# Optimization experiments

Measured on AMD Instinct MI355X. Metric: run time of the kernel, lower is better.

The kernel has to match this reference:

```python
import jax, jax.numpy as jnp
import numpy as np

B, N, NCLS = 32, 8732, 20           # batch, anchors, scored classes (bg excluded)
CONF_T, IOU_T = 0.01, 0.45
TOP_K, NMS_MAX = 200, 100
IMG_H = IMG_W = 512.0


def setup_inputs() -> dict:
    key = jax.random.key(0)
    y_pred = jax.random.uniform(key, (B, N, NCLS + 13), dtype=jnp.float32)
    return {"y_pred": y_pred}


def _decode(y):
    # SSD box decode: offsets + anchors + variances -> absolute corner coords
    scores = y[..., 1:-12]                                  # [B,N,C]
    cx_p, cy_p, w_p, h_p = y[..., -12], y[..., -11], y[..., -10], y[..., -9]
    xmin_a, ymin_a, xmax_a, ymax_a = y[..., -8], y[..., -7], y[..., -6], y[..., -5]
    w_a, h_a = xmax_a - xmin_a, ymax_a - ymin_a
    cx_a, cy_a = (xmax_a + xmin_a) * 0.5, (ymax_a + ymin_a) * 0.5
    vcx, vcy, vw, vh = y[..., -4], y[..., -3], y[..., -2], y[..., -1]
    cx = cx_p * vcx * w_a + cx_a
    cy = cy_p * vcy * h_a + cy_a
    w = jnp.exp(w_p * vw) * w_a
    h = jnp.exp(h_p * vh) * h_a
    xmin = (cx - 0.5 * w) * IMG_W
    ymin = (cy - 0.5 * h) * IMG_H
    xmax = (cx + 0.5 * w) * IMG_W
    ymax = (cy + 0.5 * h) * IMG_H
    boxes = jnp.stack([xmin, ymin, xmax, ymax], axis=-1)    # [B,N,4]
    return boxes, scores


def _select(boxes, scores):
    # Greedy per-class NMS. boxes [N,4], scores [N] (-inf below threshold).
    # Returns (indices into original box order, validity) of length NMS_MAX.
    n = scores.shape[0]
    order = jnp.argsort(-scores)
    b = boxes[order]
    s = scores[order]
    area = jnp.maximum(b[:, 2] - b[:, 0], 0.0) * jnp.maximum(b[:, 3] - b[:, 1], 0.0)
    idx_range = jnp.arange(n)

    def step(suppressed, _):
        avail = (~suppressed) & (s > -jnp.inf)
        i = jnp.argmax(avail)            # first unsuppressed box in score order
        has = avail[i]
        box = b[i]
        ix1 = jnp.maximum(box[0], b[:, 0])
        iy1 = jnp.maximum(box[1], b[:, 1])
        ix2 = jnp.minimum(box[2], b[:, 2])
        iy2 = jnp.minimum(box[3], b[:, 3])
        inter = jnp.maximum(ix2 - ix1, 0.0) * jnp.maximum(iy2 - iy1, 0.0)
        iou = inter / (area[i] + area - inter + 1e-9)
        suppressed = suppressed | (has & (iou > IOU_T)) | (idx_range == i)
        return suppressed, (order[i], has)

    _, (sel, valid) = jax.lax.scan(step, jnp.zeros(n, bool), None, length=NMS_MAX)
    return sel, valid


def _forward(y_pred):
    boxes, scores = _decode(y_pred)                          # [B,N,4], [B,N,C]
    s_thr = jnp.where(scores > CONF_T, scores, -jnp.inf)
    s_bcn = jnp.transpose(s_thr, (0, 2, 1))                  # [B,C,N]
    # NMS selection is index-only: run it on stop_gradient'd values
    sel, valid = jax.vmap(jax.vmap(_select, in_axes=(None, 0)), in_axes=(0, 0))(
        jax.lax.stop_gradient(boxes), jax.lax.stop_gradient(s_bcn))  # [B,C,M]
    Bv, C, M = sel.shape
    batch_ix = jnp.arange(Bv)
    sel_scores = jnp.take_along_axis(s_bcn, sel, axis=2)     # [B,C,M]
    sel_boxes = boxes[batch_ix[:, None, None], sel]          # [B,C,M,4]
    masked = jnp.where(valid, sel_scores, -jnp.inf)
    flat_s = masked.reshape(Bv, C * M)
    flat_b = sel_boxes.reshape(Bv, C * M, 4)
    flat_v = valid.reshape(Bv, C * M)
    _, top_idx = jax.lax.top_k(jax.lax.stop_gradient(flat_s), TOP_K)  # [B,TOP_K]
    g_s = jnp.take_along_axis(flat_s, top_idx, axis=1)
    g_v = jnp.take_along_axis(flat_v, top_idx, axis=1)
    g_b = flat_b[batch_ix[:, None], top_idx]                 # [B,TOP_K,4]
    cls = (top_idx // M).astype(jnp.float32)
    cls_out = jnp.where(g_v, cls, 0.0) + 1.0                 # layer does nmsed_class += 1
    score_out = jnp.where(g_v, g_s, 0.0)
    box_out = jnp.where(g_v[..., None], g_b, 0.0)
    return jnp.concatenate([cls_out[..., None], score_out[..., None], box_out], axis=-1)


def reference(y_pred):
    return _forward(y_pred)  # [B, TOP_K, 6]: [class_id, conf, xmin, ymin, xmax, ymax]
```

## Files before the change

kernel.cpp:

```cpp
#include <hip/hip_runtime.h>
#include <cmath>

#define BB 32
#define NN 8732
#define NCLS 20
#define NCH 33
#define NMSM 100
#define TOPK 200
#define CAND (NCLS*NMSM)
#define APB 256
#define NBLK_B ((NN + APB - 1)/APB)
#define NBUCK 2048
#define CCAP 256
#define CMIN 192
#define TBUCK 4096
#define TCMIN 200

typedef unsigned long long u64;
typedef unsigned int u32;

__device__ __forceinline__ u64 shfl_xor_u64(u64 v, int m) {
  u32 lo = (u32)v, hi = (u32)(v >> 32);
  lo = (u32)__shfl_xor((int)lo, m, 64);
  hi = (u32)__shfl_xor((int)hi, m, 64);
  return ((u64)hi << 32) | (u64)lo;
}

__global__ __launch_bounds__(256)
void decode_kernel(const float* __restrict__ y,
                   float4* __restrict__ boxes,
                   float* __restrict__ scores_t) {
  __shared__ float ly[APB * NCH];
  int blk = blockIdx.x;
  int b = blk / NBLK_B, chunk = blk % NBLK_B;
  int a0 = chunk * APB;
  int na = min(APB, NN - a0);
  const float4* src4 = (const float4*)(y + ((size_t)b * NN + a0) * NCH);
  float4* ly4 = (float4*)ly;
  int nf4 = na * NCH / 4;
  for (int k = threadIdx.x; k < nf4; k += 256) ly4[k] = src4[k];
  __syncthreads();
  int t = threadIdx.x;
  if (t < na) {
    const float* p = ly + t * NCH;
    #pragma unroll
    for (int c = 0; c < NCLS; c++)
      scores_t[((size_t)b * NCLS + c) * NN + a0 + t] = p[1 + c];
    float cx_p = p[21], cy_p = p[22], w_p = p[23], h_p = p[24];
    float xmin_a = p[25], ymin_a = p[26], xmax_a = p[27], ymax_a = p[28];
    float vcx = p[29], vcy = p[30], vw = p[31], vh = p[32];
    float w_a = xmax_a - xmin_a, h_a = ymax_a - ymin_a;
    float cx_a = (xmax_a + xmin_a) * 0.5f, cy_a = (ymax_a + ymin_a) * 0.5f;
    float cx = cx_p * vcx * w_a + cx_a;
    float cy = cy_p * vcy * h_a + cy_a;
    float w = expf(w_p * vw) * w_a;
    float h = expf(h_p * vh) * h_a;
    float4 bxv;
    bxv.x = (cx - 0.5f * w) * 512.0f;
    bxv.y = (cy - 0.5f * h) * 512.0f;
    bxv.z = (cx + 0.5f * w) * 512.0f;
    bxv.w = (cy + 0.5f * h) * 512.0f;
    boxes[b * NN + a0 + t] = bxv;
  }
}

__global__ __launch_bounds__(256)
void nms_kernel(const float4* __restrict__ boxes,
                const float* __restrict__ scores_t,
                float* __restrict__ sel_score,
                float4* __restrict__ sel_box) {
  __shared__ u32 hist[NBUCK];
  __shared__ u32 chunks[256];
  __shared__ u64 ckey[CCAP];
  __shared__ float4 lbox[CCAP];
  __shared__ float lar[CCAP];
  __shared__ u64 sel_k[NMSM];
  __shared__ int sel_g[NMSM];
  __shared__ int s_cnt, s_bstar, s_nsel;

  int bc = blockIdx.x, b = bc / NCLS;
  const float* sc = scores_t + (size_t)bc * NN;
  const float4* bx = boxes + (size_t)b * NN;
  int tid = threadIdx.x, lane = tid & 63, wid = tid >> 6;

  for (int k = tid; k < NBUCK; k += 256) hist[k] = 0;
  if (tid == 0) s_cnt = 0;
  __syncthreads();

  {
    const float4* sc4 = (const float4*)sc;
    for (int n = tid; n < NN / 4; n += 256) {
      float4 v = sc4[n];
      if (v.x > 0.01f) atomicAdd(&hist[min((int)(v.x * (float)NBUCK), NBUCK - 1)], 1u);
      if (v.y > 0.01f) atomicAdd(&hist[min((int)(v.y * (float)NBUCK), NBUCK - 1)], 1u);
      if (v.z > 0.01f) atomicAdd(&hist[min((int)(v.z * (float)NBUCK), NBUCK - 1)], 1u);
      if (v.w > 0.01f) atomicAdd(&hist[min((int)(v.w * (float)NBUCK), NBUCK - 1)], 1u);
    }
  }
  __syncthreads();
  {
    u32 cs = 0;
    #pragma unroll
    for (int q = 0; q < 8; q++) cs += hist[tid * 8 + q];
    chunks[tid] = cs;
  }
  __syncthreads();
  if (tid == 0) {
    int acc = 0, bstar = 0;
    for (int c2 = 255; c2 >= 0; c2--) {
      int na2 = acc + (int)chunks[c2];
      if (na2 >= CMIN) {
        for (int q = 7; q >= 0; q--) {
          acc += (int)hist[c2 * 8 + q];
          if (acc >= CMIN) { bstar = c2 * 8 + q; break; }
        }
        break;
      }
      acc = na2;
    }
    s_bstar = bstar;
  }
  __syncthreads();
  int bstar = s_bstar;

  for (int n = tid; n < NN; n += 256) {
    float s = sc[n];
    bool q = false;
    if (s > 0.01f) q = (min((int)(s * (float)NBUCK), NBUCK - 1) >= bstar);
    u64 mask = __ballot(q);
    if (mask) {
      int leader = __ffsll(mask) - 1;
      int base = 0;
      if (q && lane == leader) base = atomicAdd(&s_cnt, __popcll(mask));
      base = __shfl(base, leader);
      if (q) {
        int pos = base + __popcll(mask & ((1ULL << lane) - 1ULL));
        if (pos < CCAP)
          ckey[pos] = ((u64)__float_as_uint(s) << 32) | (u64)(0xFFFFFFFFu - (u32)n);
      }
    }
  }
  __syncthreads();
  if (tid >= min(s_cnt, CCAP)) ckey[tid] = 0ULL;
  __syncthreads();

  u64 key[4];
  if (wid == 0) {
    #pragma unroll
    for (int s = 0; s < 4; s++) key[s] = ckey[4 * lane + s];
    for (int k = 2; k <= CCAP; k <<= 1) {
      for (int j = k >> 1; j >= 4; j >>= 1) {
        int lm = j >> 2;
        #pragma unroll
        for (int s = 0; s < 4; s++) {
          u64 pk = shfl_xor_u64(key[s], lm);
          int g = 4 * lane + s;
          bool lower = (g & j) == 0;
          bool desc = (g & k) == 0;
          bool keepmax = (desc == lower);
          u64 mx = (key[s] > pk) ? key[s] : pk;
          u64 mn = (key[s] > pk) ? pk : key[s];
          key[s] = keepmax ? mx : mn;
        }
      }
      if (k >= 4) {
        #pragma unroll
        for (int s = 0; s < 2; s++) {
          int g = 4 * lane + s;
          bool desc = (g & k) == 0;
          u64 a = key[s], c2 = key[s + 2];
          u64 mx = (a > c2) ? a : c2, mn = (a > c2) ? c2 : a;
          key[s] = desc ? mx : mn; key[s + 2] = desc ? mn : mx;
        }
      }
      {
        #pragma unroll
        for (int s = 0; s < 4; s += 2) {
          int g = 4 * lane + s;
          bool desc = (g & k) == 0;
          u64 a = key[s], c2 = key[s + 1];
          u64 mx = (a > c2) ? a : c2, mn = (a > c2) ? c2 : a;
          key[s] = desc ? mx : mn; key[s + 1] = desc ? mn : mx;
        }
      }
    }
    #pragma unroll
    for (int s = 0; s < 4; s++) ckey[4 * lane + s] = key[s];
  }
  __syncthreads();

  {
    u64 g = ckey[tid];
    float4 bb = make_float4(0.f, 0.f, 0.f, 0.f);
    if (g) bb = bx[(int)(0xFFFFFFFFu - (u32)g)];
    lbox[tid] = bb;
    lar[tid] = fmaxf(bb.z - bb.x, 0.f) * fmaxf(bb.w - bb.y, 0.f);
  }
  __syncthreads();

  if (wid == 0) {
    float X1[4], Y1[4], X2[4], Y2[4], AR[4];
    u32 am = 0, dg = 0;
    #pragma unroll
    for (int s = 0; s < 4; s++) {
      int g = 4 * lane + s;
      float4 bb = lbox[g];
      X1[s] = bb.x; Y1[s] = bb.y; X2[s] = bb.z; Y2[s] = bb.w;
      AR[s] = lar[g];
      if (key[s]) am |= (1u << s);
      if (!(AR[s] > 0.f)) dg |= (1u << s);
    }
    int nsel = 0;
    #pragma unroll 1
    for (int m = 0; m < NMSM; m++) {
      u64 bal = __ballot(am != 0u);
      if (bal == 0ULL) break;
      int w = __ffsll(bal) - 1;
      int sl_ = (__ffs(am) - 1) & 3;
      u32 pk = (u32)sl_ | (((dg >> sl_) & 1u) << 2);
      u32 pkw = (u32)__shfl((int)pk, w, 64);
      int slw = (int)(pkw & 3u);
      int g = (w << 2) + slw;
      if (lane == w) {
        am &= ~(1u << slw);
        u64 kk = key[0];
        if (slw == 1) kk = key[1];
        if (slw == 2) kk = key[2];
        if (slw == 3) kk = key[3];
        sel_k[m] = kk;
        sel_g[m] = g;
      }
      nsel = m + 1;
      if ((pkw & 4u) == 0u) {
        float4 sb = lbox[g];
        float sa = lar[g];
        #pragma unroll
        for (int s = 0; s < 4; s++) {
          float ix1 = fmaxf(sb.x, X1[s]), iy1 = fmaxf(sb.y, Y1[s]);
          float ix2 = fminf(sb.z, X2[s]), iy2 = fminf(sb.w, Y2[s]);
          float inter = fmaxf(ix2 - ix1, 0.f) * fmaxf(iy2 - iy1, 0.f);
          float iou = inter / (sa + AR[s] - inter + 1e-9f);
          if (iou > 0.45f) am &= ~(1u << s);
        }
      }
    }
    if (lane == 0) s_nsel = nsel;
  }
  __syncthreads();

  int nsel = s_nsel;
  if (tid < NMSM) {
    if (tid < nsel) {
      u64 kk = sel_k[tid];
      sel_score[(size_t)bc * NMSM + tid] = __uint_as_float((u32)(kk >> 32));
      sel_box[(size_t)bc * NMSM + tid] = lbox[sel_g[tid]];
    } else {
      sel_score[(size_t)bc * NMSM + tid] = -INFINITY;
    }
  }
}

__global__ __launch_bounds__(512)
void topk_kernel(const float* __restrict__ sel_score,
                 const float4* __restrict__ sel_box,
                 float* __restrict__ out) {
  __shared__ float lsc[CAND];
  __shared__ u32 hist[TBUCK];
  __shared__ u64 ckey[512];
  __shared__ u32 chunks[512];
  __shared__ int s_cnt, s_bstar;
  int b = blockIdx.x;
  int tid = threadIdx.x;
  int lane = tid & 63;

  for (int k = tid; k < TBUCK; k += 512) hist[k] = 0;
  if (tid == 0) s_cnt = 0;
  __syncthreads();
  for (int t = tid; t < CAND; t += 512) {
    float s = sel_score[(size_t)b * CAND + t];
    lsc[t] = s;
    if (s > 0.f) atomicAdd(&hist[min((int)(s * (float)TBUCK), TBUCK - 1)], 1u);
  }
  __syncthreads();
  {
    u32 cs = 0;
    #pragma unroll
    for (int q = 0; q < 8; q++) cs += hist[tid * 8 + q];
    chunks[tid] = cs;
  }
  __syncthreads();
  if (tid == 0) {
    int acc = 0, bstar = 0;
    for (int c2 = 511; c2 >= 0; c2--) {
      int na = acc + (int)chunks[c2];
      if (na >= TCMIN) {
        for (int q = 7; q >= 0; q--) {
          acc += (int)hist[c2 * 8 + q];
          if (acc >= TCMIN) { bstar = c2 * 8 + q; break; }
        }
        break;
      }
      acc = na;
    }
    s_bstar = bstar;
  }
  __syncthreads();
  int bstar = s_bstar;
  for (int t = tid; t < CAND; t += 512) {
    float s = lsc[t];
    bool q = false;
    if (s > 0.f) q = (min((int)(s * (float)TBUCK), TBUCK - 1) >= bstar);
    u64 mask = __ballot(q);
    if (mask) {
      int leader = __ffsll(mask) - 1;
      int base = 0;
      if (q && lane == leader) base = atomicAdd(&s_cnt, __popcll(mask));
      base = __shfl(base, leader);
      if (q) {
        int pos = base + __popcll(mask & ((1ULL << lane) - 1ULL));
        if (pos < 512)
          ckey[pos] = ((u64)__float_as_uint(s) << 32) | (u64)(0xFFFFFFFFu - (u32)t);
      }
    }
  }
  __syncthreads();
  int C = min(s_cnt, 512);
  for (int k = C + tid; k < 512; k += 512) ckey[k] = 0ULL;
  __syncthreads();

  for (int kk = 2; kk <= 512; kk <<= 1) {
    for (int j = kk >> 1; j > 0; j >>= 1) {
      int t = tid;
      int ixj = t ^ j;
      if (ixj > t && t < 512) {
        u64 a = ckey[t], c2 = ckey[ixj];
        bool desc = ((t & kk) == 0);
        if (desc ? (a < c2) : (a > c2)) { ckey[t] = c2; ckey[ixj] = a; }
      }
      __syncthreads();
    }
  }

  for (int k = tid; k < TOPK; k += 512) {
    u64 g = ckey[k];
    float o0 = 1.0f, o1 = 0.0f;
    float4 bb = make_float4(0.f, 0.f, 0.f, 0.f);
    if (g != 0ULL) {
      int flat = (int)(0xFFFFFFFFu - (u32)g);
      o0 = (float)(flat / NMSM) + 1.0f;
      o1 = __uint_as_float((u32)(g >> 32));
      bb = sel_box[(size_t)b * CAND + flat];
    }
    float* op = out + ((size_t)b * TOPK + k) * 6;
    op[0] = o0; op[1] = o1; op[2] = bb.x; op[3] = bb.y; op[4] = bb.z; op[5] = bb.w;
  }
}

extern "C" void kernel_launch(void* const* d_in, const int* in_sizes, int n_in,
                              void* d_out, int out_size, void* d_ws, size_t ws_size,
                              hipStream_t stream) {
  const float* y = (const float*)d_in[0];
  float* out = (float*)d_out;
  char* ws = (char*)d_ws;

  size_t boxesB = (size_t)BB * NN * 16;
  size_t scoresB = (size_t)BB * NCLS * NN * 4;
  size_t selScoreB = (size_t)BB * CAND * 4;

  float4* boxes    = (float4*)ws;
  float* scores_t  = (float*)(ws + boxesB);
  float* sel_score = (float*)(ws + boxesB + scoresB);
  float4* sel_box  = (float4*)(ws + boxesB + scoresB + selScoreB);

  decode_kernel<<<BB * NBLK_B, 256, 0, stream>>>(y, boxes, scores_t);
  nms_kernel<<<BB * NCLS, 256, 0, stream>>>(boxes, scores_t, sel_score, sel_box);
  topk_kernel<<<BB, 512, 0, stream>>>(sel_score, sel_box, out);
}
```

Measured before the change: 143.4 us.

## Decode boxes lazily for NMS candidates and keep scores in registers

Box decoding moves out of the first kernel, so no full boxes buffer is written and read back. Each NMS block decodes boxes only for its up-to-256 candidates, reading them straight from the raw input. The score row is now loaded once into registers and reused for both the histogram and compaction passes instead of being read from global memory twice. A shfl is also replaced with readlane. In exchange, boxes are decoded redundantly across classes and per-candidate strided gathers of 12 floats are added, along with more register pressure from the 9 float4 values.

```diff
diff --git a/kernel.cpp b/kernel.cpp
--- a/kernel.cpp
+++ b/kernel.cpp
@@ -13,6 +13,7 @@
 #define NBUCK 2048
 #define CCAP 256
 #define CMIN 192
+#define NF4 (NN/4)
 #define TBUCK 4096
 #define TCMIN 200
 
@@ -27,9 +28,8 @@
 }
 
 __global__ __launch_bounds__(256)
-void decode_kernel(const float* __restrict__ y,
-                   float4* __restrict__ boxes,
-                   float* __restrict__ scores_t) {
+void transpose_kernel(const float* __restrict__ y,
+                      float* __restrict__ scores_t) {
   __shared__ float ly[APB * NCH];
   int blk = blockIdx.x;
   int b = blk / NBLK_B, chunk = blk % NBLK_B;
@@ -46,26 +46,11 @@
     #pragma unroll
     for (int c = 0; c < NCLS; c++)
       scores_t[((size_t)b * NCLS + c) * NN + a0 + t] = p[1 + c];
-    float cx_p = p[21], cy_p = p[22], w_p = p[23], h_p = p[24];
-    float xmin_a = p[25], ymin_a = p[26], xmax_a = p[27], ymax_a = p[28];
-    float vcx = p[29], vcy = p[30], vw = p[31], vh = p[32];
-    float w_a = xmax_a - xmin_a, h_a = ymax_a - ymin_a;
-    float cx_a = (xmax_a + xmin_a) * 0.5f, cy_a = (ymax_a + ymin_a) * 0.5f;
-    float cx = cx_p * vcx * w_a + cx_a;
-    float cy = cy_p * vcy * h_a + cy_a;
-    float w = expf(w_p * vw) * w_a;
-    float h = expf(h_p * vh) * h_a;
-    float4 bxv;
-    bxv.x = (cx - 0.5f * w) * 512.0f;
-    bxv.y = (cy - 0.5f * h) * 512.0f;
-    bxv.z = (cx + 0.5f * w) * 512.0f;
-    bxv.w = (cy + 0.5f * h) * 512.0f;
-    boxes[b * NN + a0 + t] = bxv;
   }
 }
 
 __global__ __launch_bounds__(256)
-void nms_kernel(const float4* __restrict__ boxes,
+void nms_kernel(const float* __restrict__ y,
                 const float* __restrict__ scores_t,
                 float* __restrict__ sel_score,
                 float4* __restrict__ sel_box) {
@@ -80,21 +65,26 @@
 
   int bc = blockIdx.x, b = bc / NCLS;
   const float* sc = scores_t + (size_t)bc * NN;
-  const float4* bx = boxes + (size_t)b * NN;
   int tid = threadIdx.x, lane = tid & 63, wid = tid >> 6;
 
   for (int k = tid; k < NBUCK; k += 256) hist[k] = 0;
   if (tid == 0) s_cnt = 0;
   __syncthreads();
 
+  float4 v[9];
   {
     const float4* sc4 = (const float4*)sc;
-    for (int n = tid; n < NN / 4; n += 256) {
-      float4 v = sc4[n];
-      if (v.x > 0.01f) atomicAdd(&hist[min((int)(v.x * (float)NBUCK), NBUCK - 1)], 1u);
-      if (v.y > 0.01f) atomicAdd(&hist[min((int)(v.y * (float)NBUCK), NBUCK - 1)], 1u);
-      if (v.z > 0.01f) atomicAdd(&hist[min((int)(v.z * (float)NBUCK), NBUCK - 1)], 1u);
-      if (v.w > 0.01f) atomicAdd(&hist[min((int)(v.w * (float)NBUCK), NBUCK - 1)], 1u);
+    #pragma unroll
+    for (int s = 0; s < 9; s++) {
+      int n4 = tid + s * 256;
+      v[s] = (n4 < NF4) ? sc4[n4] : make_float4(0.f, 0.f, 0.f, 0.f);
+    }
+    #pragma unroll
+    for (int s = 0; s < 9; s++) {
+      if (v[s].x > 0.01f) atomicAdd(&hist[min((int)(v[s].x * (float)NBUCK), NBUCK - 1)], 1u);
+      if (v[s].y > 0.01f) atomicAdd(&hist[min((int)(v[s].y * (float)NBUCK), NBUCK - 1)], 1u);
+      if (v[s].z > 0.01f) atomicAdd(&hist[min((int)(v[s].z * (float)NBUCK), NBUCK - 1)], 1u);
+      if (v[s].w > 0.01f) atomicAdd(&hist[min((int)(v[s].w * (float)NBUCK), NBUCK - 1)], 1u);
     }
   }
   __syncthreads();
@@ -123,20 +113,26 @@
   __syncthreads();
   int bstar = s_bstar;
 
-  for (int n = tid; n < NN; n += 256) {
-    float s = sc[n];
-    bool q = false;
-    if (s > 0.01f) q = (min((int)(s * (float)NBUCK), NBUCK - 1) >= bstar);
-    u64 mask = __ballot(q);
-    if (mask) {
-      int leader = __ffsll(mask) - 1;
-      int base = 0;
-      if (q && lane == leader) base = atomicAdd(&s_cnt, __popcll(mask));
-      base = __shfl(base, leader);
-      if (q) {
-        int pos = base + __popcll(mask & ((1ULL << lane) - 1ULL));
-        if (pos < CCAP)
-          ckey[pos] = ((u64)__float_as_uint(s) << 32) | (u64)(0xFFFFFFFFu - (u32)n);
+  #pragma unroll
+  for (int s = 0; s < 9; s++) {
+    #pragma unroll
+    for (int c4 = 0; c4 < 4; c4++) {
+      float sv = (c4 == 0) ? v[s].x : (c4 == 1) ? v[s].y : (c4 == 2) ? v[s].z : v[s].w;
+      int n = (tid + s * 256) * 4 + c4;
+      bool q = false;
+      if (sv > 0.01f && n < NN)
+        q = (min((int)(sv * (float)NBUCK), NBUCK - 1) >= bstar);
+      u64 mask = __ballot(q);
+      if (mask) {
+        int leader = __ffsll(mask) - 1;
+        int base = 0;
+        if (q && lane == leader) base = atomicAdd(&s_cnt, __popcll(mask));
+        base = __shfl(base, leader);
+        if (q) {
+          int pos = base + __popcll(mask & ((1ULL << lane) - 1ULL));
+          if (pos < CCAP)
+            ckey[pos] = ((u64)__float_as_uint(sv) << 32) | (u64)(0xFFFFFFFFu - (u32)n);
+        }
       }
     }
   }
@@ -192,7 +188,23 @@
   {
     u64 g = ckey[tid];
     float4 bb = make_float4(0.f, 0.f, 0.f, 0.f);
-    if (g) bb = bx[(int)(0xFFFFFFFFu - (u32)g)];
+    if (g) {
+      int n = (int)(0xFFFFFFFFu - (u32)g);
+      const float* p = y + ((size_t)b * NN + n) * NCH;
+      float cx_p = p[21], cy_p = p[22], w_p = p[23], h_p = p[24];
+      float xmin_a = p[25], ymin_a = p[26], xmax_a = p[27], ymax_a = p[28];
+      float vcx = p[29], vcy = p[30], vw = p[31], vh = p[32];
+      float w_a = xmax_a - xmin_a, h_a = ymax_a - ymin_a;
+      float cx_a = (xmax_a + xmin_a) * 0.5f, cy_a = (ymax_a + ymin_a) * 0.5f;
+      float cx = cx_p * vcx * w_a + cx_a;
+      float cy = cy_p * vcy * h_a + cy_a;
+      float w = expf(w_p * vw) * w_a;
+      float h = expf(h_p * vh) * h_a;
+      bb.x = (cx - 0.5f * w) * 512.0f;
+      bb.y = (cy - 0.5f * h) * 512.0f;
+      bb.z = (cx + 0.5f * w) * 512.0f;
+      bb.w = (cy + 0.5f * h) * 512.0f;
+    }
     lbox[tid] = bb;
     lar[tid] = fmaxf(bb.z - bb.x, 0.f) * fmaxf(bb.w - bb.y, 0.f);
   }
@@ -218,7 +230,7 @@
       int w = __ffsll(bal) - 1;
       int sl_ = (__ffs(am) - 1) & 3;
       u32 pk = (u32)sl_ | (((dg >> sl_) & 1u) << 2);
-      u32 pkw = (u32)__shfl((int)pk, w, 64);
+      u32 pkw = (u32)__builtin_amdgcn_readlane((int)pk, w);
       int slw = (int)(pkw & 3u);
       int g = (w << 2) + slw;
       if (lane == w) {
@@ -363,16 +375,14 @@
   float* out = (float*)d_out;
   char* ws = (char*)d_ws;
 
-  size_t boxesB = (size_t)BB * NN * 16;
   size_t scoresB = (size_t)BB * NCLS * NN * 4;
   size_t selScoreB = (size_t)BB * CAND * 4;
 
-  float4* boxes    = (float4*)ws;
-  float* scores_t  = (float*)(ws + boxesB);
-  float* sel_score = (float*)(ws + boxesB + scoresB);
-  float4* sel_box  = (float4*)(ws + boxesB + scoresB + selScoreB);
-
-  decode_kernel<<<BB * NBLK_B, 256, 0, stream>>>(y, boxes, scores_t);
-  nms_kernel<<<BB * NCLS, 256, 0, stream>>>(boxes, scores_t, sel_score, sel_box);
+  float* scores_t  = (float*)ws;
+  float* sel_score = (float*)(ws + scoresB);
+  float4* sel_box  = (float4*)(ws + scoresB + selScoreB);
+
+  transpose_kernel<<<BB * NBLK_B, 256, 0, stream>>>(y, scores_t);
+  nms_kernel<<<BB * NCLS, 256, 0, stream>>>(y, scores_t, sel_score, sel_box);
   topk_kernel<<<BB, 512, 0, stream>>>(sel_score, sel_box, out);
 }
```

After: 137.2 us. 4.3% less time.
